# Kernel tuning notes

Hardware: AMD Instinct MI355X
Metric: run time of the kernel (lower is better)

Reference implementation:

```python
import jax, jax.numpy as jnp
import numpy as np


def setup_inputs() -> dict:
    key = jax.random.key(0)
    ks = jax.random.split(key, 5)
    B, C_in, C_out, E, H, W = 32, 256, 256, 8, 56, 56
    Ch = C_in // 4
    x = jax.random.normal(ks[0], (B, C_in, H, W), dtype=jnp.float32)
    # expert kernel bank, stored [E, C_out, C_in] (1x1 kernels)
    weights = jax.random.normal(ks[1], (E, C_out, C_in), dtype=jnp.float32) * (1.0 / np.sqrt(C_in))
    # attention generator: 1x1 convs == linear layers on pooled features
    w1 = jax.random.normal(ks[2], (Ch, C_in), dtype=jnp.float32) * (1.0 / np.sqrt(C_in))
    b1 = jnp.zeros((Ch,), dtype=jnp.float32)
    w2 = jax.random.normal(ks[3], (E, Ch), dtype=jnp.float32) * (1.0 / np.sqrt(Ch))
    b2 = jnp.zeros((E,), dtype=jnp.float32)
    return {"x": x, "weights": weights, "w1": w1, "b1": b1, "w2": w2, "b2": b2}


def reference(x, weights, w1, b1, w2, b2):
    # x: [B, C_in, H, W]; weights: [E, C_out, C_in]
    # attn_generator: global avg pool -> 1x1 conv -> relu -> 1x1 conv
    pooled = jnp.mean(x, axis=(2, 3))                      # [B, C_in]
    h = jax.nn.relu(pooled @ w1.T + b1)                    # [B, C_in//4]
    logits = h @ w2.T + b2                                 # [B, E]
    attn = jax.nn.softmax(logits, axis=1)                  # softmax over experts
    # per-sample fused 1x1 kernel: sum_e attn[b,e] * weights[e]
    w_dyn = jnp.einsum('be,eoc->boc', attn, weights)       # [B, C_out, C_in]
    # grouped 1x1 conv with groups=B == per-sample matmul over channels
    out = jnp.einsum('boc,bchw->bohw', w_dyn, x)           # [B, C_out, H, W]
    return out
```

## Files before the change

kernel.cpp:

```cpp
#include <hip/hip_runtime.h>

typedef unsigned short u16;
typedef __attribute__((ext_vector_type(8))) short short8;
typedef __attribute__((ext_vector_type(4))) float floatx4;

__device__ __forceinline__ u16 f32_to_bf16_rne(float f) {
  union { float f; unsigned int u; } v; v.f = f;
  unsigned int u = v.u;
  u += 0x7FFFu + ((u >> 16) & 1u);
  return (u16)(u >> 16);
}

__device__ __forceinline__ void load_lds_16(const void* gsrc, void* lds) {
  __builtin_amdgcn_global_load_lds(
      (const __attribute__((address_space(1))) unsigned int*)gsrc,
      (__attribute__((address_space(3))) unsigned int*)lds,
      16, 0, 0);
}

__global__ __launch_bounds__(256) void pool_kernel(const float* __restrict__ x,
                                                   float* __restrict__ pooled) {
  const int bc = blockIdx.x;
  const float4* row = (const float4*)(x + (size_t)bc * 3136);
  const int t = threadIdx.x;
  float s = 0.0f;
  for (int q = t; q < 784; q += 256) {
    float4 v = row[q];
    s += (v.x + v.y) + (v.z + v.w);
  }
  #pragma unroll
  for (int off = 32; off > 0; off >>= 1) s += __shfl_down(s, off, 64);
  __shared__ float red[4];
  if ((t & 63) == 0) red[t >> 6] = s;
  __syncthreads();
  if (t == 0) pooled[bc] = (red[0] + red[1] + red[2] + red[3]) * (1.0f / 3136.0f);
}

__global__ __launch_bounds__(256) void attn_wdyn_kernel(
    const float* __restrict__ pooled, const float* __restrict__ weights,
    const float* __restrict__ w1, const float* __restrict__ b1,
    const float* __restrict__ w2, const float* __restrict__ b2,
    u16* __restrict__ wdyn) {
  const int blk = blockIdx.x;
  const int b = blk >> 3;
  const int oc = blk & 7;
  const int t = threadIdx.x;
  __shared__ float ph[256];
  __shared__ float hb[64];
  __shared__ float lg[8];
  ph[t] = pooled[b * 256 + t];
  __syncthreads();
  if (t < 64) {
    float acc = b1[t];
    const float* wr = w1 + t * 256;
    for (int c = 0; c < 256; ++c) acc += ph[c] * wr[c];
    hb[t] = fmaxf(acc, 0.0f);
  }
  __syncthreads();
  if (t < 8) {
    float acc = b2[t];
    const float* wr = w2 + t * 64;
    for (int j = 0; j < 64; ++j) acc += hb[j] * wr[j];
    lg[t] = acc;
  }
  __syncthreads();
  float a[8];
  {
    float mx = lg[0];
    #pragma unroll
    for (int e = 1; e < 8; ++e) mx = fmaxf(mx, lg[e]);
    float sum = 0.0f;
    #pragma unroll
    for (int e = 0; e < 8; ++e) { a[e] = __expf(lg[e] - mx); sum += a[e]; }
    float inv = 1.0f / sum;
    #pragma unroll
    for (int e = 0; e < 8; ++e) a[e] *= inv;
  }
  const int o0 = oc * 32;
  for (int i = 0; i < 32; ++i) {
    const int o = o0 + i;
    float acc = 0.0f;
    #pragma unroll
    for (int e = 0; e < 8; ++e)
      acc += a[e] * weights[((size_t)e * 256 + o) * 256 + t];
    wdyn[((size_t)b * 256 + o) * 256 + t] = f32_to_bf16_rne(acc);
  }
}

#define BM 128
#define BN 64
#define BK 32
#define XP 40

__global__ __launch_bounds__(256) void dynconv_gemm(const float* __restrict__ x,
                                                    const u16* __restrict__ wdyn,
                                                    float* __restrict__ out) {
  const int nb = blockIdx.x;
  const int mb = blockIdx.y;
  const int b  = blockIdx.z;
  const int t = threadIdx.x;
  const int lane = t & 63;
  const int wv = t >> 6;
  const int quad = lane >> 4;
  const int l16 = lane & 15;

  __shared__ u16 Ws[BM * BK];
  __shared__ u16 Xs[BN * XP];

  const float* xb = x + (size_t)b * (256 * 3136);
  const u16* wb = wdyn + ((size_t)b * 256 + mb * BM) * 256;
  float* ob = out + ((size_t)b * 256 + mb * BM) * 3136;
  const int n0 = nb * BN;

  floatx4 acc[2][4];
  #pragma unroll
  for (int i = 0; i < 2; ++i)
    #pragma unroll
    for (int j = 0; j < 4; ++j) acc[i][j] = (floatx4)(0.0f);

  const int xn = lane;
  const int xkg = wv;

  for (int kt = 0; kt < 8; ++kt) {
    const int k0 = kt * BK;
    #pragma unroll
    for (int j = 0; j < 2; ++j) {
      const int i = j * 256 + t;
      const int r = i >> 2;
      const int c8 = i & 3;
      load_lds_16(wb + r * 256 + k0 + c8 * 8, &Ws[i * 8]);
    }
    {
      const float* xs = xb + (size_t)(k0 + xkg * 8) * 3136 + n0 + xn;
      short8 pk;
      #pragma unroll
      for (int j = 0; j < 8; ++j) {
        pk[j] = (short)f32_to_bf16_rne(xs[(size_t)j * 3136]);
      }
      *(short8*)(&Xs[xn * XP + xkg * 8]) = pk;
    }
    __syncthreads();
    short8 af[2];
    #pragma unroll
    for (int mt = 0; mt < 2; ++mt) {
      const int r = wv * 32 + mt * 16 + l16;
      af[mt] = *(const short8*)(&Ws[r * BK + quad * 8]);
    }
    short8 bfr[4];
    #pragma unroll
    for (int nt = 0; nt < 4; ++nt) {
      const int n = nt * 16 + l16;
      bfr[nt] = *(const short8*)(&Xs[n * XP + quad * 8]);
    }
    #pragma unroll
    for (int mt = 0; mt < 2; ++mt)
      #pragma unroll
      for (int nt = 0; nt < 4; ++nt)
        acc[mt][nt] = __builtin_amdgcn_mfma_f32_16x16x32_bf16(
            af[mt], bfr[nt], acc[mt][nt], 0, 0, 0);
    __syncthreads();
  }
  #pragma unroll
  for (int mt = 0; mt < 2; ++mt) {
    const int orow = wv * 32 + mt * 16 + quad * 4;
    #pragma unroll
    for (int nt = 0; nt < 4; ++nt) {
      const int n = n0 + nt * 16 + l16;
      #pragma unroll
      for (int r = 0; r < 4; ++r)
        ob[(size_t)(orow + r) * 3136 + n] = acc[mt][nt][r];
    }
  }
}

extern "C" void kernel_launch(void* const* d_in, const int* in_sizes, int n_in,
                              void* d_out, int out_size, void* d_ws, size_t ws_size,
                              hipStream_t stream) {
  const float* x       = (const float*)d_in[0];
  const float* weights = (const float*)d_in[1];
  const float* w1      = (const float*)d_in[2];
  const float* b1      = (const float*)d_in[3];
  const float* w2      = (const float*)d_in[4];
  const float* b2      = (const float*)d_in[5];
  float* out = (float*)d_out;

  float* pooled = (float*)d_ws;
  u16* wdyn = (u16*)((char*)d_ws + 32768);

  pool_kernel<<<8192, 256, 0, stream>>>(x, pooled);
  attn_wdyn_kernel<<<256, 256, 0, stream>>>(pooled, weights, w1, b1, w2, b2, wdyn);
  dynconv_gemm<<<dim3(49, 2, 32), 256, 0, stream>>>(x, wdyn, out);
}
```

Before: 244.6 us.

## Cover all output channels per GEMM block and parallelize attention MLP

The GEMM tile grows from 128 to 256 output rows, so each block covers every output channel for a sample. Each x tile is then loaded and converted to bf16 once instead of twice, and the grid shrinks to 49x32 blocks. The attention MLP in attn_wdyn_kernel spreads its dot products across all threads with partial sums instead of using 64 or 8 serial threads. It also uses packed bf16 conversion intrinsics for x. The trade-off is more accumulator registers, lower occupancy and fewer blocks for the device.

```diff
diff --git a/kernel.cpp b/kernel.cpp
--- a/kernel.cpp
+++ b/kernel.cpp
@@ -1,4 +1,5 @@
 #include <hip/hip_runtime.h>
+#include <hip/hip_bf16.h>
 
 typedef unsigned short u16;
 typedef __attribute__((ext_vector_type(8))) short short8;
@@ -46,22 +47,40 @@
   const int oc = blk & 7;
   const int t = threadIdx.x;
   __shared__ float ph[256];
+  __shared__ float part[256];
   __shared__ float hb[64];
   __shared__ float lg[8];
   ph[t] = pooled[b * 256 + t];
   __syncthreads();
+  {
+    const int row = t >> 2, seg = t & 3;
+    const float* wr = w1 + row * 256 + seg * 64;
+    const float* pp = ph + seg * 64;
+    float a = 0.0f;
+    #pragma unroll 8
+    for (int c = 0; c < 64; ++c) a += pp[c] * wr[c];
+    part[t] = a;
+  }
+  __syncthreads();
   if (t < 64) {
-    float acc = b1[t];
-    const float* wr = w1 + t * 256;
-    for (int c = 0; c < 256; ++c) acc += ph[c] * wr[c];
-    hb[t] = fmaxf(acc, 0.0f);
+    float a = part[t * 4] + part[t * 4 + 1] + part[t * 4 + 2] + part[t * 4 + 3] + b1[t];
+    hb[t] = fmaxf(a, 0.0f);
+  }
+  __syncthreads();
+  if (t < 64) {
+    const int row = t >> 3, seg = t & 7;
+    const float* wr = w2 + row * 64 + seg * 8;
+    float a = 0.0f;
+    #pragma unroll
+    for (int j = 0; j < 8; ++j) a += hb[seg * 8 + j] * wr[j];
+    part[t] = a;
   }
   __syncthreads();
   if (t < 8) {
-    float acc = b2[t];
-    const float* wr = w2 + t * 64;
-    for (int j = 0; j < 64; ++j) acc += hb[j] * wr[j];
-    lg[t] = acc;
+    float a = b2[t];
+    #pragma unroll
+    for (int j = 0; j < 8; ++j) a += part[t * 8 + j];
+    lg[t] = a;
   }
   __syncthreads();
   float a[8];
@@ -87,7 +106,7 @@
   }
 }
 
-#define BM 128
+#define BM 256
 #define BN 64
 #define BK 32
 #define XP 40
@@ -96,8 +115,7 @@
                                                     const u16* __restrict__ wdyn,
                                                     float* __restrict__ out) {
   const int nb = blockIdx.x;
-  const int mb = blockIdx.y;
-  const int b  = blockIdx.z;
+  const int b  = blockIdx.y;
   const int t = threadIdx.x;
   const int lane = t & 63;
   const int wv = t >> 6;
@@ -108,13 +126,13 @@
   __shared__ u16 Xs[BN * XP];
 
   const float* xb = x + (size_t)b * (256 * 3136);
-  const u16* wb = wdyn + ((size_t)b * 256 + mb * BM) * 256;
-  float* ob = out + ((size_t)b * 256 + mb * BM) * 3136;
+  const u16* wb = wdyn + (size_t)b * 256 * 256;
+  float* ob = out + (size_t)b * 256 * 3136;
   const int n0 = nb * BN;
 
-  floatx4 acc[2][4];
+  floatx4 acc[4][4];
   #pragma unroll
-  for (int i = 0; i < 2; ++i)
+  for (int i = 0; i < 4; ++i)
     #pragma unroll
     for (int j = 0; j < 4; ++j) acc[i][j] = (floatx4)(0.0f);
 
@@ -124,7 +142,7 @@
   for (int kt = 0; kt < 8; ++kt) {
     const int k0 = kt * BK;
     #pragma unroll
-    for (int j = 0; j < 2; ++j) {
+    for (int j = 0; j < 4; ++j) {
       const int i = j * 256 + t;
       const int r = i >> 2;
       const int c8 = i & 3;
@@ -132,20 +150,19 @@
     }
     {
       const float* xs = xb + (size_t)(k0 + xkg * 8) * 3136 + n0 + xn;
+      float v[8];
+      #pragma unroll
+      for (int j = 0; j < 8; ++j) v[j] = xs[(size_t)j * 3136];
       short8 pk;
       #pragma unroll
-      for (int j = 0; j < 8; ++j) {
-        pk[j] = (short)f32_to_bf16_rne(xs[(size_t)j * 3136]);
+      for (int j = 0; j < 4; ++j) {
+        __hip_bfloat162 h2 = __float22bfloat162_rn(make_float2(v[2 * j], v[2 * j + 1]));
+        union { __hip_bfloat162 h; struct { short lo, hi; } s; } u; u.h = h2;
+        pk[2 * j] = u.s.lo; pk[2 * j + 1] = u.s.hi;
       }
       *(short8*)(&Xs[xn * XP + xkg * 8]) = pk;
     }
     __syncthreads();
-    short8 af[2];
-    #pragma unroll
-    for (int mt = 0; mt < 2; ++mt) {
-      const int r = wv * 32 + mt * 16 + l16;
-      af[mt] = *(const short8*)(&Ws[r * BK + quad * 8]);
-    }
     short8 bfr[4];
     #pragma unroll
     for (int nt = 0; nt < 4; ++nt) {
@@ -153,16 +170,19 @@
       bfr[nt] = *(const short8*)(&Xs[n * XP + quad * 8]);
     }
     #pragma unroll
-    for (int mt = 0; mt < 2; ++mt)
+    for (int mt = 0; mt < 4; ++mt) {
+      const int r = wv * 64 + mt * 16 + l16;
+      short8 af = *(const short8*)(&Ws[r * BK + quad * 8]);
       #pragma unroll
       for (int nt = 0; nt < 4; ++nt)
         acc[mt][nt] = __builtin_amdgcn_mfma_f32_16x16x32_bf16(
-            af[mt], bfr[nt], acc[mt][nt], 0, 0, 0);
+            af, bfr[nt], acc[mt][nt], 0, 0, 0);
+    }
     __syncthreads();
   }
   #pragma unroll
-  for (int mt = 0; mt < 2; ++mt) {
-    const int orow = wv * 32 + mt * 16 + quad * 4;
+  for (int mt = 0; mt < 4; ++mt) {
+    const int orow = wv * 64 + mt * 16 + quad * 4;
     #pragma unroll
     for (int nt = 0; nt < 4; ++nt) {
       const int n = n0 + nt * 16 + l16;
@@ -189,5 +209,5 @@
 
   pool_kernel<<<8192, 256, 0, stream>>>(x, pooled);
   attn_wdyn_kernel<<<256, 256, 0, stream>>>(pooled, weights, w1, b1, w2, b2, wdyn);
-  dynconv_gemm<<<dim3(49, 2, 32), 256, 0, stream>>>(x, wdyn, out);
-}
+  dynconv_gemm<<<dim3(49, 32), 256, 0, stream>>>(x, wdyn, out);
+}
```

After: 231.5 us. -5.4%, faster.
